# Kernel optimization log

Hardware: AMD Instinct MI355X
Metric: run time of the kernel (lower is better)

## Reference

```python
import jax, jax.numpy as jnp
import numpy as np

R, N, E, IN_DIM, HID, SEM_H = 3, 50000, 500000, 256, 128, 128


def setup_inputs() -> dict:
    key = jax.random.key(0)
    ks = jax.random.split(key, 20)
    s = 0.05
    return {
        # forward tensor args
        "dst_feat": jax.random.normal(ks[0], (N, IN_DIM), jnp.float32),
        "src_feats": jax.random.normal(ks[1], (R, N, IN_DIM), jnp.float32),
        "src_idx": jax.random.randint(ks[2], (R, E), 0, N, jnp.int32),
        "dst_idx": jax.random.randint(ks[3], (R, E), 0, N, jnp.int32),
        # weight_T: per-ntype projection in_dim -> hidden (dst ntype + R src ntypes, stacked)
        "WT_dst": jax.random.normal(ks[4], (IN_DIM, HID), jnp.float32) * s,
        "bT_dst": jnp.zeros((HID,), jnp.float32),
        "WT_src": jax.random.normal(ks[5], (R, IN_DIM, HID), jnp.float32) * s,
        "bT_src": jnp.zeros((R, HID), jnp.float32),
        # GATConv params per relation (1 head, shared fc for src/dst since in_feats is int)
        "W_gat": jax.random.normal(ks[6], (R, HID, HID), jnp.float32) * s,
        "attn_l": jax.random.normal(ks[7], (R, HID), jnp.float32) * s,
        "attn_r": jax.random.normal(ks[8], (R, HID), jnp.float32) * s,
        "b_gat": jnp.zeros((R, HID), jnp.float32),
        # SemanticAttention: Linear(HID,128)+tanh+Linear(128,1,no bias)
        "W1_sem": jax.random.normal(ks[9], (HID, SEM_H), jnp.float32) * s,
        "b1_sem": jnp.zeros((SEM_H,), jnp.float32),
        "w2_sem": jax.random.normal(ks[10], (SEM_H, 1), jnp.float32) * s,
    }


def reference(dst_feat, src_feats, src_idx, dst_idx,
              WT_dst, bT_dst, WT_src, bT_src,
              W_gat, attn_l, attn_r, b_gat,
              W1_sem, b1_sem, w2_sem):
    # weight_T projections (raw feat dim != hidden_dim branch)
    h_dst = dst_feat @ WT_dst + bT_dst                                  # [N, H]
    h_src = jnp.einsum('rni,rio->rno', src_feats, WT_src) + bT_src[:, None, :]  # [R, N, H]
    n_nodes = h_dst.shape[0]

    def gat(h_s_in, si, di, W, al, ar, b):
        # DGL GATConv, 1 head, eval mode (no dropout), shared fc for src/dst
        hs = h_s_in @ W                                                 # [N, H]
        hd = h_dst @ W                                                  # [N, H]
        el = (hs * al).sum(-1)                                          # [N]
        er = (hd * ar).sum(-1)                                          # [N]
        e = el[si] + er[di]                                             # [E]
        e = jnp.where(e > 0, e, 0.2 * e)                                # leaky_relu(0.2)
        # edge softmax segmented by destination node
        m = jax.ops.segment_max(e, di, num_segments=n_nodes)
        ex = jnp.exp(e - m[di])
        ssum = jax.ops.segment_sum(ex, di, num_segments=n_nodes)
        alpha = ex / ssum[di]                                           # [E]
        out = jax.ops.segment_sum(alpha[:, None] * hs[si], di, num_segments=n_nodes)  # [N, H]
        return jax.nn.elu(out + b)                                      # activation=F.elu, + bias

    z_r = jax.vmap(gat)(h_src, src_idx, dst_idx, W_gat, attn_l, attn_r, b_gat)  # [R, N, H]

    # SemanticAttention over relations
    z_m = jnp.transpose(z_r, (1, 0, 2))                                 # [N, R, H]
    w = jnp.tanh(z_m @ W1_sem + b1_sem) @ w2_sem                        # [N, R, 1]
    a = jax.nn.softmax(w.mean(axis=0), axis=0)                          # [R, 1]
    return (z_m * a).sum(axis=1)                                        # [N, H]
```

## Files before the change

kernel.cpp:

```cpp
#include <hip/hip_runtime.h>
#include <hip/hip_bf16.h>

#define R_REL 3
#define NODE_CHUNK 512
#define BCAP 6144

typedef __attribute__((ext_vector_type(8))) short bf16x8;
typedef __attribute__((ext_vector_type(4))) float f32x4;

static inline size_t align_up(size_t x, size_t a) { return (x + a - 1) & ~(a - 1); }

__device__ __forceinline__ float eluf(float x) {
    return x > 0.f ? x : (__expf(x) - 1.f);
}
__device__ __forceinline__ unsigned short f2bf(float f) {
    __hip_bfloat16 h = __float2bfloat16(f);
    return *reinterpret_cast<unsigned short*>(&h);
}
__device__ __forceinline__ unsigned pk2bf(float lo, float hi) {
    __hip_bfloat162 h = __float22bfloat162_rn(make_float2(lo, hi));
    return *reinterpret_cast<unsigned*>(&h);
}
__device__ __forceinline__ float bf2f(unsigned short h) {
    return __uint_as_float((unsigned)h << 16);
}


__global__ void vu_kernel(const float* __restrict__ W_gat, const float* __restrict__ attn_r,
                          const float* __restrict__ WT_dst, const float* __restrict__ bT_dst,
                          float* __restrict__ u, float* __restrict__ cc) {
    int r = blockIdx.x;
    int t = threadIdx.x;
    __shared__ float ar[128];
    __shared__ float vs[128];
    if (t < 128) ar[t] = attn_r[r * 128 + t];
    __syncthreads();
    if (t < 128) {
        const float* W = W_gat + (size_t)r * 128 * 128 + (size_t)t * 128;
        float s = 0.f;
        for (int j = 0; j < 128; ++j) s += W[j] * ar[j];
        vs[t] = s;
    }
    __syncthreads();
    const float* W = WT_dst + (size_t)t * 128;
    float s = 0.f;
    for (int i = 0; i < 128; ++i) s += W[i] * vs[i];
    u[r * 256 + t] = s;
    if (t == 0) {
        float c = 0.f;
        for (int i = 0; i < 128; ++i) c += bT_dst[i] * vs[i];
        cc[r] = c;
    }
}

__global__ void wc_kernel(const float* __restrict__ WT_src, const float* __restrict__ bT_src,
                          const float* __restrict__ W_gat, float* __restrict__ Wc,
                          float* __restrict__ bc) {
    int r = blockIdx.y;
    int k = blockIdx.x;
    int j = threadIdx.x;
    __shared__ float as[128];
    const float* arow = (k < 256) ? (WT_src + ((size_t)r * 256 + k) * 128)
                                  : (bT_src + (size_t)r * 128);
    as[j] = arow[j];
    __syncthreads();
    const float* W = W_gat + (size_t)r * 128 * 128;
    float s = 0.f;
    for (int i = 0; i < 128; ++i) s += as[i] * W[(size_t)i * 128 + j];
    if (k < 256) Wc[((size_t)r * 256 + k) * 128 + j] = s;
    else         bc[(size_t)r * 128 + j] = s;
}

__global__ void pack_kernel(const float* __restrict__ S, unsigned short* __restrict__ P,
                            int relstride, int KS) {
    int r = blockIdx.y;
    int ks = blockIdx.x >> 3, cb = blockIdx.x & 7;
    int l = threadIdx.x;
    const float* Sr = S + (size_t)r * relstride;
    int col = cb * 16 + (l & 15);
    int kb = ks * 32 + (l >> 4) * 8;
    unsigned short v[8];
#pragma unroll
    for (int j = 0; j < 8; ++j) v[j] = f2bf(Sr[(size_t)(kb + j) * 128 + col]);
    unsigned short* dst = P + ((((size_t)r * KS + ks) * 8 + cb) * 64 + l) * 8;
    *(uint4*)dst = *(uint4*)v;
}


__global__ __launch_bounds__(1024) void gemm_hs(
    const float* __restrict__ src, const unsigned short* __restrict__ Bpack,
    const float* __restrict__ bc, const float* __restrict__ attn_l,
    unsigned short* __restrict__ hsb, float* __restrict__ el, int N) {
    const int r = blockIdx.y;
    const int t = threadIdx.x;
    const int w = t >> 6, l = t & 63;
    __shared__ unsigned short Blds[256 * 128];

    const unsigned short* bsrc = Bpack + (size_t)r * 256 * 128;
#pragma unroll
    for (int i = 0; i < 4; ++i) {
        int c = i * 1024 + t;
        *(uint4*)&Blds[(size_t)c * 8] = *(const uint4*)&bsrc[(size_t)c * 8];
    }
    __syncthreads();

    const int rowbase = blockIdx.x * 256 + w * 16;
    const int arow_i = rowbase + (l & 15);
    const int kg = l >> 4;
    const float* A = src + (size_t)r * N * 256;
    const float* arow = A + (size_t)(arow_i < N ? arow_i : N - 1) * 256;

    f32x4 acc[8] = {};
#pragma unroll
    for (int ks = 0; ks < 8; ++ks) {
        float4 a0 = *(const float4*)(arow + ks * 32 + kg * 8);
        float4 a1 = *(const float4*)(arow + ks * 32 + kg * 8 + 4);
        uint4 uv;
        uv.x = pk2bf(a0.x, a0.y);
        uv.y = pk2bf(a0.z, a0.w);
        uv.z = pk2bf(a1.x, a1.y);
        uv.w = pk2bf(a1.z, a1.w);
        bf16x8 av = *(bf16x8*)&uv;
#pragma unroll
        for (int cf = 0; cf < 8; ++cf) {
            bf16x8 bv = *(const bf16x8*)&Blds[((size_t)(ks * 8 + cf) * 64 + l) * 8];
            acc[cf] = __builtin_amdgcn_mfma_f32_16x16x32_bf16(av, bv, acc[cf], 0, 0, 0);
        }
    }
    float bcv[8], alv[8];
#pragma unroll
    for (int cf = 0; cf < 8; ++cf) {
        int col = cf * 16 + (l & 15);
        bcv[cf] = bc[r * 128 + col];
        alv[cf] = attn_l[r * 128 + col];
    }
#pragma unroll
    for (int i = 0; i < 4; ++i) {
        int row = rowbase + (l >> 4) * 4 + i;
        float pe = 0.f;
        unsigned short hv[8];
#pragma unroll
        for (int cf = 0; cf < 8; ++cf) {
            float v = acc[cf][i] + bcv[cf];
            pe += v * alv[cf];
            hv[cf] = f2bf(v);
        }
        if (row < N) {
            unsigned short* hp = hsb + ((size_t)r * N + row) * 128 + (l & 15);
#pragma unroll
            for (int cf = 0; cf < 8; ++cf) hp[cf * 16] = hv[cf];
        }
        pe += __shfl_xor(pe, 1, 64);
        pe += __shfl_xor(pe, 2, 64);
        pe += __shfl_xor(pe, 4, 64);
        pe += __shfl_xor(pe, 8, 64);
        if ((l & 15) == 0 && row < N) el[(size_t)r * N + row] = pe;
    }
}


__global__ void er_kernel(const float* __restrict__ dst_feat, const float* __restrict__ u,
                          const float* __restrict__ cc, float* __restrict__ er, int N) {
    __shared__ float us[3][256];
    for (int i = threadIdx.x; i < 3 * 256; i += 256) us[i / 256][i & 255] = u[i];
    __syncthreads();
    int wave = threadIdx.x >> 6, lane = threadIdx.x & 63;
    int n = blockIdx.x * 4 + wave;
    if (n >= N) return;
    float4 f = *(const float4*)(dst_feat + (size_t)n * 256 + lane * 4);
#pragma unroll
    for (int r = 0; r < R_REL; ++r) {
        float4 uv = *(float4*)&us[r][lane * 4];
        float s = f.x * uv.x + f.y * uv.y + f.z * uv.z + f.w * uv.w;
#pragma unroll
        for (int off = 32; off >= 1; off >>= 1) s += __shfl_xor(s, off, 64);
        if (lane == 0) er[(size_t)r * N + n] = s + cc[r];
    }
}


__global__ __launch_bounds__(256) void bucket_kernel(
    const int* __restrict__ si, const int* __restrict__ di,
    int* __restrict__ gcnt, unsigned* __restrict__ bbuf, int NB, int E) {
    const int r = blockIdx.y;
    const int t = threadIdx.x;
    const int e0 = blockIdx.x * 1024;
    __shared__ int cnt[128];
    __shared__ int base[128];
    if (t < 128) cnt[t] = 0;
    __syncthreads();
    int bk[4], rank[4]; unsigned pack[4]; bool val[4];
#pragma unroll
    for (int j = 0; j < 4; ++j) {
        int e = e0 + j * 256 + t;
        val[j] = e < E;
        bk[j] = 0; rank[j] = 0; pack[j] = 0;
        if (val[j]) {
            size_t g = (size_t)r * E + e;
            int s = si[g], d = di[g];
            bk[j] = d >> 9;
            pack[j] = (unsigned)s | ((unsigned)d << 16);
            rank[j] = atomicAdd(&cnt[bk[j]], 1);
        }
    }
    __syncthreads();
    if (t < NB && cnt[t] > 0) base[t] = atomicAdd(&gcnt[r * NB + t], cnt[t]);
    __syncthreads();
#pragma unroll
    for (int j = 0; j < 4; ++j) {
        if (val[j])
            bbuf[((size_t)r * NB + bk[j]) * BCAP + base[bk[j]] + rank[j]] = pack[j];
    }
}

__global__ void bscan_kernel(const int* __restrict__ gcnt, int* __restrict__ bbase, int NB) {
    int r = threadIdx.x;
    if (r >= R_REL) return;
    int acc = 0;
    for (int i = 0; i < NB; ++i) {
        bbase[r * NB + i] = acc;
        acc += gcnt[r * NB + i];
    }
}

__global__ __launch_bounds__(256) void fill3_kernel(
    const unsigned* __restrict__ bbuf, const int* __restrict__ gcnt,
    const int* __restrict__ bbase, const float* __restrict__ el, const float* __restrict__ er,
    int* __restrict__ offs, int* __restrict__ deg, uint2* __restrict__ epair,
    int NB, int N, int E) {
    const int r = blockIdx.y;
    const int b = blockIdx.x;
    const int t = threadIdx.x;
    const int lane = t & 63, wave = t >> 6;
    __shared__ int hist[NODE_CHUNK];
    __shared__ int curl[NODE_CHUNK];
    __shared__ float erl[NODE_CHUNK];
    __shared__ int wsum[4];
    __shared__ int wpre[4];

    for (int i = t; i < NODE_CHUNK; i += 256) hist[i] = 0;
    {
        int idx0 = b * NODE_CHUNK + t;
        int idx1 = idx0 + 256;
        erl[t]       = (idx0 < N) ? er[(size_t)r * N + idx0] : 0.f;
        erl[t + 256] = (idx1 < N) ? er[(size_t)r * N + idx1] : 0.f;
    }
    __syncthreads();

    const int cnt = gcnt[r * NB + b];
    const int bb0 = bbase[r * NB + b];
    const unsigned* bb = bbuf + ((size_t)r * NB + b) * BCAP;

    for (int i = t; i < cnt; i += 256) {
        int dloc = (bb[i] >> 16) & (NODE_CHUNK - 1);
        atomicAdd(&hist[dloc], 1);
    }
    __syncthreads();

    int a0 = hist[2 * t], a1 = hist[2 * t + 1];
    int s = a0 + a1;
    int x = s;
#pragma unroll
    for (int off = 1; off < 64; off <<= 1) {
        int y = __shfl_up(x, off, 64);
        if (lane >= off) x += y;
    }
    if (lane == 63) wsum[wave] = x;
    __syncthreads();
    if (t == 0) {
        int acc = 0;
#pragma unroll
        for (int w2 = 0; w2 < 4; ++w2) { wpre[w2] = acc; acc += wsum[w2]; }
    }
    __syncthreads();
    int excl = wpre[wave] + x - s;
    curl[2 * t] = excl;
    curl[2 * t + 1] = excl + a0;
    {
        int idx0 = b * NODE_CHUNK + 2 * t;
        if (idx0 < N) { offs[(size_t)r * N + idx0] = bb0 + excl; deg[(size_t)r * N + idx0] = a0; }
        int idx1 = idx0 + 1;
        if (idx1 < N) { offs[(size_t)r * N + idx1] = bb0 + excl + a0; deg[(size_t)r * N + idx1] = a1; }
    }
    __syncthreads();

    const float* elr = el + (size_t)r * N;
    uint2* epr = epair + (size_t)r * E;
    for (int i = t; i < cnt; i += 256) {
        unsigned pk = bb[i];
        int src = pk & 0xffffu;
        int dloc = (pk >> 16) & (NODE_CHUNK - 1);
        float e = elr[src] + erl[dloc];
        e = e > 0.f ? e : 0.2f * e;
        float p = __expf(e);
        int pos = bb0 + atomicAdd(&curl[dloc], 1);
        epr[pos] = make_uint2((unsigned)src, __float_as_uint(p));
    }
}


__global__ __launch_bounds__(256) void gather_kernel(
    const uint2* __restrict__ epair, const int* __restrict__ offs,
    const int* __restrict__ deg, const unsigned short* __restrict__ hsb,
    const float* __restrict__ b_gat, unsigned short* __restrict__ z, int N, int E) {
    const int r = blockIdx.y;
    const int t = threadIdx.x;
    const int gid = t >> 4;
    const int gl = t & 15;
    const int d = blockIdx.x * 16 + gid;
    if (d >= N) return;
    const int beg = offs[(size_t)r * N + d];
    const int dg = deg[(size_t)r * N + d];
    float ac[8] = {0.f, 0.f, 0.f, 0.f, 0.f, 0.f, 0.f, 0.f};
    float ssum = 0.f;
    const uint2* epr = epair + (size_t)r * E;
    const unsigned short* hsr = hsb + (size_t)r * N * 128;
    int i = beg;
    const int end = beg + dg;
    for (; i + 3 < end; i += 4) {
        uint2 v0 = epr[i], v1 = epr[i + 1], v2 = epr[i + 2], v3 = epr[i + 3];
        uint4 h0 = *(const uint4*)(hsr + (size_t)v0.x * 128 + gl * 8);
        uint4 h1 = *(const uint4*)(hsr + (size_t)v1.x * 128 + gl * 8);
        uint4 h2 = *(const uint4*)(hsr + (size_t)v2.x * 128 + gl * 8);
        uint4 h3 = *(const uint4*)(hsr + (size_t)v3.x * 128 + gl * 8);
        float p0 = __uint_as_float(v0.y), p1 = __uint_as_float(v1.y);
        float p2 = __uint_as_float(v2.y), p3 = __uint_as_float(v3.y);
        ssum += p0 + p1 + p2 + p3;
        ac[0] += p0 * bf2f((unsigned short)(h0.x & 0xffffu)) + p1 * bf2f((unsigned short)(h1.x & 0xffffu))
               + p2 * bf2f((unsigned short)(h2.x & 0xffffu)) + p3 * bf2f((unsigned short)(h3.x & 0xffffu));
        ac[1] += p0 * bf2f((unsigned short)(h0.x >> 16)) + p1 * bf2f((unsigned short)(h1.x >> 16))
               + p2 * bf2f((unsigned short)(h2.x >> 16)) + p3 * bf2f((unsigned short)(h3.x >> 16));
        ac[2] += p0 * bf2f((unsigned short)(h0.y & 0xffffu)) + p1 * bf2f((unsigned short)(h1.y & 0xffffu))
               + p2 * bf2f((unsigned short)(h2.y & 0xffffu)) + p3 * bf2f((unsigned short)(h3.y & 0xffffu));
        ac[3] += p0 * bf2f((unsigned short)(h0.y >> 16)) + p1 * bf2f((unsigned short)(h1.y >> 16))
               + p2 * bf2f((unsigned short)(h2.y >> 16)) + p3 * bf2f((unsigned short)(h3.y >> 16));
        ac[4] += p0 * bf2f((unsigned short)(h0.z & 0xffffu)) + p1 * bf2f((unsigned short)(h1.z & 0xffffu))
               + p2 * bf2f((unsigned short)(h2.z & 0xffffu)) + p3 * bf2f((unsigned short)(h3.z & 0xffffu));
        ac[5] += p0 * bf2f((unsigned short)(h0.z >> 16)) + p1 * bf2f((unsigned short)(h1.z >> 16))
               + p2 * bf2f((unsigned short)(h2.z >> 16)) + p3 * bf2f((unsigned short)(h3.z >> 16));
        ac[6] += p0 * bf2f((unsigned short)(h0.w & 0xffffu)) + p1 * bf2f((unsigned short)(h1.w & 0xffffu))
               + p2 * bf2f((unsigned short)(h2.w & 0xffffu)) + p3 * bf2f((unsigned short)(h3.w & 0xffffu));
        ac[7] += p0 * bf2f((unsigned short)(h0.w >> 16)) + p1 * bf2f((unsigned short)(h1.w >> 16))
               + p2 * bf2f((unsigned short)(h2.w >> 16)) + p3 * bf2f((unsigned short)(h3.w >> 16));
    }
    for (; i < end; ++i) {
        uint2 v = epr[i];
        float p = __uint_as_float(v.y);
        ssum += p;
        uint4 hw = *(const uint4*)(hsr + (size_t)v.x * 128 + gl * 8);
        ac[0] += p * bf2f((unsigned short)(hw.x & 0xffffu));
        ac[1] += p * bf2f((unsigned short)(hw.x >> 16));
        ac[2] += p * bf2f((unsigned short)(hw.y & 0xffffu));
        ac[3] += p * bf2f((unsigned short)(hw.y >> 16));
        ac[4] += p * bf2f((unsigned short)(hw.z & 0xffffu));
        ac[5] += p * bf2f((unsigned short)(hw.z >> 16));
        ac[6] += p * bf2f((unsigned short)(hw.w & 0xffffu));
        ac[7] += p * bf2f((unsigned short)(hw.w >> 16));
    }
    float inv = (dg > 0) ? 1.f / ssum : 0.f;
    const float* bg = b_gat + r * 128 + gl * 8;
    uint4 ow;
    ow.x = pk2bf(eluf(ac[0] * inv + bg[0]), eluf(ac[1] * inv + bg[1]));
    ow.y = pk2bf(eluf(ac[2] * inv + bg[2]), eluf(ac[3] * inv + bg[3]));
    ow.z = pk2bf(eluf(ac[4] * inv + bg[4]), eluf(ac[5] * inv + bg[5]));
    ow.w = pk2bf(eluf(ac[6] * inv + bg[6]), eluf(ac[7] * inv + bg[7]));
    *(uint4*)(z + ((size_t)r * N + d) * 128 + gl * 8) = ow;
}


__global__ __launch_bounds__(256) void gemm_sem(
    const unsigned short* __restrict__ z, const unsigned short* __restrict__ W1p,
    const float* __restrict__ b1, const float* __restrict__ w2,
    float* __restrict__ wpart, int N) {
    const int r = blockIdx.y;
    const int n0 = blockIdx.x * 64;
    const int t = threadIdx.x;
    const int w = t >> 6, l = t & 63;
    __shared__ unsigned short Alds[64 * 128];
    __shared__ float sred[4];
    const unsigned short* A = z + (size_t)r * N * 128;
#pragma unroll
    for (int i = 0; i < 4; ++i) {
        int cid = t + 256 * i;
        int row = cid >> 4, kc = cid & 15;
        uint4 v = make_uint4(0, 0, 0, 0);
        if (n0 + row < N) v = *(const uint4*)(A + (size_t)(n0 + row) * 128 + kc * 8);
        int off = ((row * 256) + kc * 16) ^ ((row & 7) << 4);
        *(uint4*)((char*)Alds + off) = v;
    }
    __syncthreads();

    const bf16x8* bp = (const bf16x8*)W1p;
    f32x4 acc[8] = {};
    const int arow = w * 16 + (l & 15);
#pragma unroll
    for (int ks = 0; ks < 4; ++ks) {
        int aoff = ((arow * 256) + ks * 64 + (l >> 4) * 16) ^ ((arow & 7) << 4);
        bf16x8 av = *(const bf16x8*)((char*)Alds + aoff);
#pragma unroll
        for (int cf = 0; cf < 8; ++cf) {
            bf16x8 bv = bp[(ks * 8 + cf) * 64 + l];
            acc[cf] = __builtin_amdgcn_mfma_f32_16x16x32_bf16(av, bv, acc[cf], 0, 0, 0);
        }
    }
    float b1v[8], w2v[8];
#pragma unroll
    for (int cf = 0; cf < 8; ++cf) {
        int col = cf * 16 + (l & 15);
        b1v[cf] = b1[col];
        w2v[cf] = w2[col];
    }
    float wloc = 0.f;
#pragma unroll
    for (int i = 0; i < 4; ++i) {
        int row = n0 + w * 16 + (l >> 4) * 4 + i;
        float s = 0.f;
#pragma unroll
        for (int cf = 0; cf < 8; ++cf) s += tanhf(acc[cf][i] + b1v[cf]) * w2v[cf];
        s += __shfl_xor(s, 1, 64);
        s += __shfl_xor(s, 2, 64);
        s += __shfl_xor(s, 4, 64);
        s += __shfl_xor(s, 8, 64);
        if ((l & 15) == 0 && row < N) wloc += s;
    }
    wloc += __shfl_xor(wloc, 16, 64);
    wloc += __shfl_xor(wloc, 32, 64);
    if (l == 0) sred[w] = wloc;
    __syncthreads();
    if (t == 0)
        wpart[(size_t)r * gridDim.x + blockIdx.x] = sred[0] + sred[1] + sred[2] + sred[3];
}


__global__ void reduce_sem(const float* __restrict__ wpart, float* __restrict__ aw,
                           int nblk, int N) {
    const int t = threadIdx.x, l = t & 63, w = t >> 6;
    __shared__ float sred[R_REL][4];
    float s[R_REL] = {0.f, 0.f, 0.f};
    for (int i = t; i < nblk; i += 256) {
#pragma unroll
        for (int r = 0; r < R_REL; ++r) s[r] += wpart[(size_t)r * nblk + i];
    }
#pragma unroll
    for (int r = 0; r < R_REL; ++r) {
#pragma unroll
        for (int off = 32; off >= 1; off >>= 1) s[r] += __shfl_xor(s[r], off, 64);
        if (l == 0) sred[r][w] = s[r];
    }
    __syncthreads();
    if (t == 0) {
        float w0 = (sred[0][0] + sred[0][1] + sred[0][2] + sred[0][3]) / (float)N;
        float w1 = (sred[1][0] + sred[1][1] + sred[1][2] + sred[1][3]) / (float)N;
        float w2 = (sred[2][0] + sred[2][1] + sred[2][2] + sred[2][3]) / (float)N;
        float m = fmaxf(w0, fmaxf(w1, w2));
        float e0 = __expf(w0 - m), e1 = __expf(w1 - m), e2 = __expf(w2 - m);
        float si = e0 + e1 + e2;
        aw[0] = e0 / si; aw[1] = e1 / si; aw[2] = e2 / si;
    }
}

__global__ void combine(const unsigned short* __restrict__ z, const float* __restrict__ aw,
                        float* __restrict__ out, int N) {
    int idx = blockIdx.x * 256 + threadIdx.x;
    if (idx >= N * 32) return;
    int n = idx >> 5, c4 = idx & 31;
    float a0 = aw[0], a1 = aw[1], a2 = aw[2];
    uint2 z0 = *(const uint2*)(z + ((size_t)0 * N + n) * 128 + c4 * 4);
    uint2 z1 = *(const uint2*)(z + ((size_t)1 * N + n) * 128 + c4 * 4);
    uint2 z2 = *(const uint2*)(z + ((size_t)2 * N + n) * 128 + c4 * 4);
    float4 o;
    o.x = a0 * bf2f((unsigned short)(z0.x & 0xffffu)) + a1 * bf2f((unsigned short)(z1.x & 0xffffu)) + a2 * bf2f((unsigned short)(z2.x & 0xffffu));
    o.y = a0 * bf2f((unsigned short)(z0.x >> 16))     + a1 * bf2f((unsigned short)(z1.x >> 16))     + a2 * bf2f((unsigned short)(z2.x >> 16));
    o.z = a0 * bf2f((unsigned short)(z0.y & 0xffffu)) + a1 * bf2f((unsigned short)(z1.y & 0xffffu)) + a2 * bf2f((unsigned short)(z2.y & 0xffffu));
    o.w = a0 * bf2f((unsigned short)(z0.y >> 16))     + a1 * bf2f((unsigned short)(z1.y >> 16))     + a2 * bf2f((unsigned short)(z2.y >> 16));
    *(float4*)(out + (size_t)idx * 4) = o;
}


extern "C" void kernel_launch(void* const* d_in, const int* in_sizes, int n_in,
                              void* d_out, int out_size, void* d_ws, size_t ws_size,
                              hipStream_t stream) {
    const float* dst_feat = (const float*)d_in[0];
    const float* src_feats = (const float*)d_in[1];
    const int*   src_idx  = (const int*)d_in[2];
    const int*   dst_idx  = (const int*)d_in[3];
    const float* WT_dst   = (const float*)d_in[4];
    const float* bT_dst   = (const float*)d_in[5];
    const float* WT_src   = (const float*)d_in[6];
    const float* bT_src   = (const float*)d_in[7];
    const float* W_gat    = (const float*)d_in[8];
    const float* attn_l   = (const float*)d_in[9];
    const float* attn_r   = (const float*)d_in[10];
    const float* b_gat    = (const float*)d_in[11];
    const float* W1_sem   = (const float*)d_in[12];
    const float* b1_sem   = (const float*)d_in[13];
    const float* w2_sem   = (const float*)d_in[14];

    const int N = in_sizes[0] / 256;
    const int E = in_sizes[2] / R_REL;
    float* out = (float*)d_out;

    const int nblk = (N + 63) / 64;
    const int nblk_hs = (N + 255) / 256;
    const int NB = (N + NODE_CHUNK - 1) / NODE_CHUNK;

    char* ws = (char*)d_ws;
    size_t off = 0;
    auto alloc = [&](size_t bytes) { char* p = ws + off; off = align_up(off + bytes, 256); return p; };
    unsigned short* hsb   = (unsigned short*)alloc((size_t)R_REL * N * 128 * 2);
    unsigned short* zbuf  = (unsigned short*)alloc((size_t)R_REL * N * 128 * 2);
    float*    Wc    = (float*)alloc((size_t)R_REL * 256 * 128 * 4);
    unsigned short* Wcp   = (unsigned short*)alloc((size_t)R_REL * 256 * 128 * 2);
    unsigned short* W1p   = (unsigned short*)alloc((size_t)128 * 128 * 2);
    float*    bc    = (float*)alloc(R_REL * 128 * 4);
    float*    u     = (float*)alloc(R_REL * 256 * 4);
    float*    cc    = (float*)alloc(R_REL * 4);
    float*    el    = (float*)alloc((size_t)R_REL * N * 4);
    float*    er    = (float*)alloc((size_t)R_REL * N * 4);
    int*      deg   = (int*)alloc((size_t)R_REL * N * 4);
    int*      offs  = (int*)alloc((size_t)R_REL * N * 4);
    int*      gcnt  = (int*)alloc((size_t)R_REL * NB * 4);
    int*      bbase = (int*)alloc((size_t)R_REL * NB * 4);
    unsigned* bbuf  = (unsigned*)alloc((size_t)R_REL * NB * BCAP * 4);
    uint2*    epair = (uint2*)alloc((size_t)R_REL * E * 8);
    float*    wpart = (float*)alloc((size_t)R_REL * nblk * 4);
    float*    aw    = (float*)alloc(R_REL * 4);

    hipMemsetAsync(gcnt, 0, (size_t)R_REL * NB * 4, stream);

    vu_kernel<<<R_REL, 256, 0, stream>>>(W_gat, attn_r, WT_dst, bT_dst, u, cc);
    wc_kernel<<<dim3(257, R_REL), 128, 0, stream>>>(WT_src, bT_src, W_gat, Wc, bc);
    pack_kernel<<<dim3(64, R_REL), 64, 0, stream>>>(Wc, Wcp, 256 * 128, 8);
    pack_kernel<<<dim3(32, 1), 64, 0, stream>>>(W1_sem, W1p, 0, 4);

    gemm_hs<<<dim3(nblk_hs, R_REL), 1024, 0, stream>>>(src_feats, Wcp, bc, attn_l, hsb, el, N);
    er_kernel<<<(N + 3) / 4, 256, 0, stream>>>(dst_feat, u, cc, er, N);

    bucket_kernel<<<dim3((E + 1023) / 1024, R_REL), 256, 0, stream>>>(src_idx, dst_idx, gcnt, bbuf, NB, E);
    bscan_kernel<<<1, 64, 0, stream>>>(gcnt, bbase, NB);
    fill3_kernel<<<dim3(NB, R_REL), 256, 0, stream>>>(bbuf, gcnt, bbase, el, er, offs, deg, epair, NB, N, E);

    gather_kernel<<<dim3((N + 15) / 16, R_REL), 256, 0, stream>>>(epair, offs, deg, hsb, b_gat, zbuf, N, E);

    gemm_sem<<<dim3(nblk, R_REL), 256, 0, stream>>>(zbuf, W1p, b1_sem, w2_sem, wpart, N);
    reduce_sem<<<1, 256, 0, stream>>>(wpart, aw, nblk, N);
    combine<<<(N * 32 + 255) / 256, 256, 0, stream>>>(zbuf, aw, out, N);
}
```

Measured before the change: 244.3 us.

## Halve gemm_hs block and LDS with K-split weight staging; deepen gather unroll

gemm_hs now uses 512-thread blocks covering 128 rows each and stages the packed weight matrix in two K halves of 32 KB LDS instead of one 64 KB load. The aim is higher occupancy and more blocks per CU, at the cost of an extra barrier pair and twice the total weight reloads across the grid. Separately, the gather kernel gets an 8-edge unrolled loop that issues all index and feature loads before accumulating, to raise memory-level parallelism. The wider unroll adds register pressure.

```diff
diff --git a/kernel.cpp b/kernel.cpp
--- a/kernel.cpp
+++ b/kernel.cpp
@@ -87,24 +87,17 @@
 }
 
 
-__global__ __launch_bounds__(1024) void gemm_hs(
+__global__ __launch_bounds__(512) void gemm_hs(
     const float* __restrict__ src, const unsigned short* __restrict__ Bpack,
     const float* __restrict__ bc, const float* __restrict__ attn_l,
     unsigned short* __restrict__ hsb, float* __restrict__ el, int N) {
     const int r = blockIdx.y;
     const int t = threadIdx.x;
     const int w = t >> 6, l = t & 63;
-    __shared__ unsigned short Blds[256 * 128];
+    __shared__ unsigned short Blds[128 * 128];
 
     const unsigned short* bsrc = Bpack + (size_t)r * 256 * 128;
-#pragma unroll
-    for (int i = 0; i < 4; ++i) {
-        int c = i * 1024 + t;
-        *(uint4*)&Blds[(size_t)c * 8] = *(const uint4*)&bsrc[(size_t)c * 8];
-    }
-    __syncthreads();
-
-    const int rowbase = blockIdx.x * 256 + w * 16;
+    const int rowbase = blockIdx.x * 128 + w * 16;
     const int arow_i = rowbase + (l & 15);
     const int kg = l >> 4;
     const float* A = src + (size_t)r * N * 256;
@@ -112,19 +105,31 @@
 
     f32x4 acc[8] = {};
 #pragma unroll
-    for (int ks = 0; ks < 8; ++ks) {
-        float4 a0 = *(const float4*)(arow + ks * 32 + kg * 8);
-        float4 a1 = *(const float4*)(arow + ks * 32 + kg * 8 + 4);
-        uint4 uv;
-        uv.x = pk2bf(a0.x, a0.y);
-        uv.y = pk2bf(a0.z, a0.w);
-        uv.z = pk2bf(a1.x, a1.y);
-        uv.w = pk2bf(a1.z, a1.w);
-        bf16x8 av = *(bf16x8*)&uv;
-#pragma unroll
-        for (int cf = 0; cf < 8; ++cf) {
-            bf16x8 bv = *(const bf16x8*)&Blds[((size_t)(ks * 8 + cf) * 64 + l) * 8];
-            acc[cf] = __builtin_amdgcn_mfma_f32_16x16x32_bf16(av, bv, acc[cf], 0, 0, 0);
+    for (int half = 0; half < 2; ++half) {
+        const unsigned short* hsrc = bsrc + half * 128 * 128;
+        __syncthreads();
+#pragma unroll
+        for (int i = 0; i < 4; ++i) {
+            int c = i * 512 + t;
+            *(uint4*)&Blds[(size_t)c * 8] = *(const uint4*)&hsrc[(size_t)c * 8];
+        }
+        __syncthreads();
+#pragma unroll
+        for (int ks2 = 0; ks2 < 4; ++ks2) {
+            const int ks = half * 4 + ks2;
+            float4 a0 = *(const float4*)(arow + ks * 32 + kg * 8);
+            float4 a1 = *(const float4*)(arow + ks * 32 + kg * 8 + 4);
+            uint4 uv;
+            uv.x = pk2bf(a0.x, a0.y);
+            uv.y = pk2bf(a0.z, a0.w);
+            uv.z = pk2bf(a1.x, a1.y);
+            uv.w = pk2bf(a1.z, a1.w);
+            bf16x8 av = *(bf16x8*)&uv;
+#pragma unroll
+            for (int cf = 0; cf < 8; ++cf) {
+                bf16x8 bv = *(const bf16x8*)&Blds[((size_t)(ks2 * 8 + cf) * 64 + l) * 8];
+                acc[cf] = __builtin_amdgcn_mfma_f32_16x16x32_bf16(av, bv, acc[cf], 0, 0, 0);
+            }
         }
     }
     float bcv[8], alv[8];
@@ -317,46 +322,54 @@
     const unsigned short* hsr = hsb + (size_t)r * N * 128;
     int i = beg;
     const int end = beg + dg;
+
+#define ACC_ONE(hw, p)                                                        \
+    do {                                                                      \
+        ac[0] += (p) * bf2f((unsigned short)((hw).x & 0xffffu));              \
+        ac[1] += (p) * bf2f((unsigned short)((hw).x >> 16));                  \
+        ac[2] += (p) * bf2f((unsigned short)((hw).y & 0xffffu));              \
+        ac[3] += (p) * bf2f((unsigned short)((hw).y >> 16));                  \
+        ac[4] += (p) * bf2f((unsigned short)((hw).z & 0xffffu));              \
+        ac[5] += (p) * bf2f((unsigned short)((hw).z >> 16));                  \
+        ac[6] += (p) * bf2f((unsigned short)((hw).w & 0xffffu));              \
+        ac[7] += (p) * bf2f((unsigned short)((hw).w >> 16));                  \
+    } while (0)
+
+    for (; i + 7 < end; i += 8) {
+        uint2 v[8]; uint4 h[8];
+#pragma unroll
+        for (int j = 0; j < 8; ++j) v[j] = epr[i + j];
+#pragma unroll
+        for (int j = 0; j < 8; ++j) h[j] = *(const uint4*)(hsr + (size_t)v[j].x * 128 + gl * 8);
+#pragma unroll
+        for (int j = 0; j < 8; ++j) {
+            float p = __uint_as_float(v[j].y);
+            ssum += p;
+            ACC_ONE(h[j], p);
+        }
+    }
     for (; i + 3 < end; i += 4) {
-        uint2 v0 = epr[i], v1 = epr[i + 1], v2 = epr[i + 2], v3 = epr[i + 3];
-        uint4 h0 = *(const uint4*)(hsr + (size_t)v0.x * 128 + gl * 8);
-        uint4 h1 = *(const uint4*)(hsr + (size_t)v1.x * 128 + gl * 8);
-        uint4 h2 = *(const uint4*)(hsr + (size_t)v2.x * 128 + gl * 8);
-        uint4 h3 = *(const uint4*)(hsr + (size_t)v3.x * 128 + gl * 8);
-        float p0 = __uint_as_float(v0.y), p1 = __uint_as_float(v1.y);
-        float p2 = __uint_as_float(v2.y), p3 = __uint_as_float(v3.y);
-        ssum += p0 + p1 + p2 + p3;
-        ac[0] += p0 * bf2f((unsigned short)(h0.x & 0xffffu)) + p1 * bf2f((unsigned short)(h1.x & 0xffffu))
-               + p2 * bf2f((unsigned short)(h2.x & 0xffffu)) + p3 * bf2f((unsigned short)(h3.x & 0xffffu));
-        ac[1] += p0 * bf2f((unsigned short)(h0.x >> 16)) + p1 * bf2f((unsigned short)(h1.x >> 16))
-               + p2 * bf2f((unsigned short)(h2.x >> 16)) + p3 * bf2f((unsigned short)(h3.x >> 16));
-        ac[2] += p0 * bf2f((unsigned short)(h0.y & 0xffffu)) + p1 * bf2f((unsigned short)(h1.y & 0xffffu))
-               + p2 * bf2f((unsigned short)(h2.y & 0xffffu)) + p3 * bf2f((unsigned short)(h3.y & 0xffffu));
-        ac[3] += p0 * bf2f((unsigned short)(h0.y >> 16)) + p1 * bf2f((unsigned short)(h1.y >> 16))
-               + p2 * bf2f((unsigned short)(h2.y >> 16)) + p3 * bf2f((unsigned short)(h3.y >> 16));
-        ac[4] += p0 * bf2f((unsigned short)(h0.z & 0xffffu)) + p1 * bf2f((unsigned short)(h1.z & 0xffffu))
-               + p2 * bf2f((unsigned short)(h2.z & 0xffffu)) + p3 * bf2f((unsigned short)(h3.z & 0xffffu));
-        ac[5] += p0 * bf2f((unsigned short)(h0.z >> 16)) + p1 * bf2f((unsigned short)(h1.z >> 16))
-               + p2 * bf2f((unsigned short)(h2.z >> 16)) + p3 * bf2f((unsigned short)(h3.z >> 16));
-        ac[6] += p0 * bf2f((unsigned short)(h0.w & 0xffffu)) + p1 * bf2f((unsigned short)(h1.w & 0xffffu))
-               + p2 * bf2f((unsigned short)(h2.w & 0xffffu)) + p3 * bf2f((unsigned short)(h3.w & 0xffffu));
-        ac[7] += p0 * bf2f((unsigned short)(h0.w >> 16)) + p1 * bf2f((unsigned short)(h1.w >> 16))
-               + p2 * bf2f((unsigned short)(h2.w >> 16)) + p3 * bf2f((unsigned short)(h3.w >> 16));
+        uint2 v[4]; uint4 h[4];
+#pragma unroll
+        for (int j = 0; j < 4; ++j) v[j] = epr[i + j];
+#pragma unroll
+        for (int j = 0; j < 4; ++j) h[j] = *(const uint4*)(hsr + (size_t)v[j].x * 128 + gl * 8);
+#pragma unroll
+        for (int j = 0; j < 4; ++j) {
+            float p = __uint_as_float(v[j].y);
+            ssum += p;
+            ACC_ONE(h[j], p);
+        }
     }
     for (; i < end; ++i) {
         uint2 v = epr[i];
         float p = __uint_as_float(v.y);
         ssum += p;
         uint4 hw = *(const uint4*)(hsr + (size_t)v.x * 128 + gl * 8);
-        ac[0] += p * bf2f((unsigned short)(hw.x & 0xffffu));
-        ac[1] += p * bf2f((unsigned short)(hw.x >> 16));
-        ac[2] += p * bf2f((unsigned short)(hw.y & 0xffffu));
-        ac[3] += p * bf2f((unsigned short)(hw.y >> 16));
-        ac[4] += p * bf2f((unsigned short)(hw.z & 0xffffu));
-        ac[5] += p * bf2f((unsigned short)(hw.z >> 16));
-        ac[6] += p * bf2f((unsigned short)(hw.w & 0xffffu));
-        ac[7] += p * bf2f((unsigned short)(hw.w >> 16));
-    }
+        ACC_ONE(hw, p);
+    }
+#undef ACC_ONE
+
     float inv = (dg > 0) ? 1.f / ssum : 0.f;
     const float* bg = b_gat + r * 128 + gl * 8;
     uint4 ow;
@@ -501,7 +514,7 @@
     float* out = (float*)d_out;
 
     const int nblk = (N + 63) / 64;
-    const int nblk_hs = (N + 255) / 256;
+    const int nblk_hs = (N + 127) / 128;
     const int NB = (N + NODE_CHUNK - 1) / NODE_CHUNK;
 
     char* ws = (char*)d_ws;
@@ -533,7 +546,7 @@
     pack_kernel<<<dim3(64, R_REL), 64, 0, stream>>>(Wc, Wcp, 256 * 128, 8);
     pack_kernel<<<dim3(32, 1), 64, 0, stream>>>(W1_sem, W1p, 0, 4);
 
-    gemm_hs<<<dim3(nblk_hs, R_REL), 1024, 0, stream>>>(src_feats, Wcp, bc, attn_l, hsb, el, N);
+    gemm_hs<<<dim3(nblk_hs, R_REL), 512, 0, stream>>>(src_feats, Wcp, bc, attn_l, hsb, el, N);
     er_kernel<<<(N + 3) / 4, 256, 0, stream>>>(dst_feat, u, cc, er, N);
 
     bucket_kernel<<<dim3((E + 1023) / 1024, R_REL), 256, 0, stream>>>(src_idx, dst_idx, gcnt, bbuf, NB, E);
```

Measured after the change: 244.0 us. No clear change (-0.1%).
